# Optimization experiments

Hardware: AMD Instinct MI355X
Metric: run time of the kernel (lower is better)

## Reference

```python
import jax, jax.numpy as jnp
import numpy as np

B, N, F_IN, F_OUT = 8, 2048, 256, 256
H, D = 8, 32
LN_EPS = 1e-5


def setup_inputs() -> dict:
    key = jax.random.key(0)
    ks = jax.random.split(key, 8)
    s = 1.0 / np.sqrt(F_IN)
    so = 1.0 / np.sqrt(H * D)
    return {
        "x": jax.random.normal(ks[0], (B, N, F_IN), dtype=jnp.float32),
        "adj": jax.random.randint(ks[1], (B, N, N), 0, 2, dtype=jnp.int32),
        "Wq": jax.random.uniform(ks[2], (F_IN, H * D), jnp.float32, -s, s),
        "bq": jnp.zeros((H * D,), jnp.float32),
        "Wk": jax.random.uniform(ks[3], (F_IN, H * D), jnp.float32, -s, s),
        "bk": jnp.zeros((H * D,), jnp.float32),
        "Wv": jax.random.uniform(ks[4], (F_IN, H * D), jnp.float32, -s, s),
        "bv": jnp.zeros((H * D,), jnp.float32),
        "Wo": jax.random.uniform(ks[5], (H * D, F_OUT), jnp.float32, -so, so),
        "bo": jnp.zeros((F_OUT,), jnp.float32),
        "gamma": jnp.ones((F_OUT,), jnp.float32),
        "beta": jnp.zeros((F_OUT,), jnp.float32),
    }


def reference(x, adj, Wq, bq, Wk, bk, Wv, bv, Wo, bo, gamma, beta):
    b, n, _ = x.shape
    # QKV projections -> [B, H, N, D]
    q = (x @ Wq + bq).reshape(b, n, H, D).transpose(0, 2, 1, 3)
    k = (x @ Wk + bk).reshape(b, n, H, D).transpose(0, 2, 1, 3)
    v = (x @ Wv + bv).reshape(b, n, H, D).transpose(0, 2, 1, 3)
    # masked attention scores [B, H, N, N]
    scores = jnp.einsum('bhqd,bhkd->bhqk', q, k) / np.sqrt(D).astype(np.float32)
    scores = jnp.where(adj[:, None, :, :] == 0, -jnp.inf, scores)
    attn = jax.nn.softmax(scores, axis=-1)
    # dropout layers are identity in eval mode
    out = jnp.einsum('bhqk,bhkd->bhqd', attn, v)
    out = out.transpose(0, 2, 1, 3).reshape(b, n, H * D)
    out = out @ Wo + bo
    # LayerNorm
    mu = out.mean(-1, keepdims=True)
    var = out.var(-1, keepdims=True)
    out = (out - mu) * jax.lax.rsqrt(var + LN_EPS) * gamma + beta
    return out, attn.mean(axis=1)
```

## Files before the change

### kernel.cpp

```cpp
#include <hip/hip_runtime.h>


typedef __attribute__((ext_vector_type(8))) short short8;
typedef __attribute__((ext_vector_type(4))) float f32x4;
typedef __attribute__((ext_vector_type(4))) unsigned short us4;
typedef unsigned short u16;
typedef unsigned int u32;

#define SC2 0.25503486127240555f
#define MS2 28.853900817779268f

__device__ __forceinline__ float b2f(u16 u) {
  union { u32 i; float f; } v; v.i = ((u32)u) << 16; return v.f;
}
__device__ __forceinline__ u16 f2b(float f) {
  union { float f; u32 i; } v; v.f = f;
  u32 r = v.i + 0x7FFFu + ((v.i >> 16) & 1u);
  return (u16)(r >> 16);
}
__device__ __forceinline__ u16 f2br(float f) {
  union { float f; u32 i; } v; v.f = f;
  return (u16)((v.i + 0x8000u) >> 16);
}

__global__ __launch_bounds__(256) void k_pack(const int* __restrict__ adj,
                                              u32* __restrict__ packed) {
  unsigned int i = blockIdx.x * 256u + threadIdx.x;
  unsigned long long m = __ballot(adj[i] != 0);
  int lane = threadIdx.x & 63;
  if (lane == 0)       packed[i >> 5] = (u32)m;
  else if (lane == 32) packed[i >> 5] = (u32)(m >> 32);
}

__global__ __launch_bounds__(256) void k_transpose4(
    const float* __restrict__ w0, const float* __restrict__ w1,
    const float* __restrict__ w2, const float* __restrict__ w3,
    u16* __restrict__ o0, u16* __restrict__ o1,
    u16* __restrict__ o2, u16* __restrict__ o3) {
  const float* in; u16* out;
  int z = blockIdx.z;
  if (z == 0) { in = w0; out = o0; }
  else if (z == 1) { in = w1; out = o1; }
  else if (z == 2) { in = w2; out = o2; }
  else { in = w3; out = o3; }
  __shared__ u16 t[32][33];
  int tx = threadIdx.x & 31, ty = threadIdx.x >> 5;
  int x0 = blockIdx.x * 32, y0 = blockIdx.y * 32;
  for (int j = 0; j < 32; j += 8)
    t[ty + j][tx] = f2b(in[(y0 + ty + j) * 256 + x0 + tx]);
  __syncthreads();
  for (int j = 0; j < 32; j += 8) out[(x0 + ty + j) * 256 + y0 + tx] = t[tx][ty + j];
}

__global__ __launch_bounds__(256) void k_qkv(
    const float* __restrict__ x, const u16* __restrict__ wt,
    const float* __restrict__ bq, const float* __restrict__ bk,
    const float* __restrict__ bv,
    u16* __restrict__ qw, u16* __restrict__ kw, u16* __restrict__ vt) {
  int l = threadIdx.x & 63, w = threadIdx.x >> 6;
  int lr = l & 15, lg = l >> 4;
  int row0 = blockIdx.y * 64 + w * 16;
  int c0 = blockIdx.x * 64;
  f32x4 acc[4] = {};
  const float* xr = x + (size_t)(row0 + lr) * 256 + lg * 8;
  const u16* wr = wt + (c0 + lr) * 256 + lg * 8;
  for (int k0 = 0; k0 < 256; k0 += 32) {
    f32x4 f0 = *(const f32x4*)(xr + k0);
    f32x4 f1 = *(const f32x4*)(xr + k0 + 4);
    short8 a;
    a[0] = (short)f2b(f0[0]); a[1] = (short)f2b(f0[1]);
    a[2] = (short)f2b(f0[2]); a[3] = (short)f2b(f0[3]);
    a[4] = (short)f2b(f1[0]); a[5] = (short)f2b(f1[1]);
    a[6] = (short)f2b(f1[2]); a[7] = (short)f2b(f1[3]);
#pragma unroll
    for (int ct = 0; ct < 4; ct++) {
      short8 bb = *(const short8*)(wr + ct * 16 * 256 + k0);
      acc[ct] = __builtin_amdgcn_mfma_f32_16x16x32_bf16(a, bb, acc[ct], 0, 0, 0);
    }
  }
  int mtx = blockIdx.x >> 2;
  const float* bias = (mtx == 0) ? bq : ((mtx == 1) ? bk : bv);
  int b = row0 >> 11, nbase = row0 & 2047;
#pragma unroll
  for (int ct = 0; ct < 4; ct++) {
    int cc = (c0 + ct * 16 + lr) & 255;
    int h = cc >> 5, d = cc & 31;
    float bs = bias[cc];
    if (mtx < 2) {
      u16* dst = (mtx == 0) ? qw : kw;
#pragma unroll
      for (int rr = 0; rr < 4; rr++) {
        int n = nbase + lg * 4 + rr;
        dst[((b * 8 + h) * 2048 + n) * 32 + d] = f2b(acc[ct][rr] + bs);
      }
    } else {
      us4 pk;
#pragma unroll
      for (int rr = 0; rr < 4; rr++) pk[rr] = f2b(acc[ct][rr] + bs);
      *(us4*)(vt + (size_t)((b * 8 + h) * 32 + d) * 2048 + nbase + lg * 4) = pk;
    }
  }
}

__global__ __launch_bounds__(256) void k_pass1(
    const u16* __restrict__ qw, const u16* __restrict__ kw,
    const u32* __restrict__ packed, float* __restrict__ lsl2) {
  int l = threadIdx.x & 63, w = threadIdx.x >> 6;
  int lr = l & 15, lg = l >> 4;
  int wid = blockIdx.x * 4 + w;
  int b = wid >> 9, h = (wid >> 6) & 7, q0 = (wid & 63) * 32;
  const u16* qb = qw + (size_t)((b * 8 + h) * 2048) * 32;
  const u16* kb = kw + (size_t)((b * 8 + h) * 2048) * 32;
  short8 qf0 = *(const short8*)(qb + (q0 + lr) * 32 + lg * 8);
  short8 qf1 = *(const short8*)(qb + (q0 + 16 + lr) * 32 + lg * 8);
  const u32* pkb = packed + (size_t)(b * 2048 + q0) * 64;
  float ls0 = 0.f, ls1 = 0.f;
#pragma unroll 2
  for (int ch = 0; ch < 32; ch++) {
    uint2 m0 = *(const uint2*)(pkb + lr * 64 + ch * 2);
    uint2 m1 = *(const uint2*)(pkb + (16 + lr) * 64 + ch * 2);
#pragma unroll
    for (int j = 0; j < 4; j++) {
      short8 kf = *(const short8*)(kb + (size_t)(ch * 64 + j * 16 + lr) * 32 + lg * 8);
      f32x4 z = {};
      f32x4 s0 = __builtin_amdgcn_mfma_f32_16x16x32_bf16(kf, qf0, z, 0, 0, 0);
      f32x4 s1 = __builtin_amdgcn_mfma_f32_16x16x32_bf16(kf, qf1, z, 0, 0, 0);
      u32 w0 = ((j & 2) ? m0.y : m0.x) >> ((j & 1) * 16 + lg * 4);
      u32 w1 = ((j & 2) ? m1.y : m1.x) >> ((j & 1) * 16 + lg * 4);
#pragma unroll
      for (int rr = 0; rr < 4; rr++) {
        float e0 = __builtin_exp2f(fmaf(s0[rr], SC2, -MS2));
        float e1 = __builtin_exp2f(fmaf(s1[rr], SC2, -MS2));
        ls0 += ((w0 >> rr) & 1u) ? e0 : 0.0f;
        ls1 += ((w1 >> rr) & 1u) ? e1 : 0.0f;
      }
    }
  }
  ls0 += __shfl_xor(ls0, 16); ls0 += __shfl_xor(ls0, 32);
  ls1 += __shfl_xor(ls1, 16); ls1 += __shfl_xor(ls1, 32);
  if (l < 16) {
    float* lp = lsl2 + (size_t)(b * 8 + h) * 2048 + q0;
    lp[lr]      = -__log2f(fmaxf(ls0, 1e-30f));
    lp[16 + lr] = -__log2f(fmaxf(ls1, 1e-30f));
  }
}

__global__ __launch_bounds__(512) void k_pass2(
    const u16* __restrict__ qw, const u16* __restrict__ kw,
    const u16* __restrict__ vt, const u32* __restrict__ packed,
    const float* __restrict__ lsl2, u16* __restrict__ ao,
    float* __restrict__ out2) {
  __shared__ __align__(16) u16 P[2][8][2048];
  int l = threadIdx.x & 63, h = threadIdx.x >> 6;
  int lr = l & 15, lg = l >> 4;
  int b = blockIdx.y, q0 = blockIdx.x * 32;
  const u16* qb = qw + (size_t)((b * 8 + h) * 2048 + q0) * 32;
  const u16* kb = kw + (size_t)((b * 8 + h) * 2048) * 32;
  const u16* vb = vt + (size_t)((b * 8 + h) * 32) * 2048;
  short8 qf0 = *(const short8*)(qb + lr * 32 + lg * 8);
  short8 qf1 = *(const short8*)(qb + (16 + lr) * 32 + lg * 8);
  float lil0 = lsl2[(size_t)(b * 8 + h) * 2048 + q0 + lr] - MS2;
  float lil1 = lsl2[(size_t)(b * 8 + h) * 2048 + q0 + 16 + lr] - MS2;
  f32x4 acc[2][2] = {};
  const u32* pkb = packed + (size_t)(b * 2048 + q0) * 64;
  for (int ch = 0; ch < 32; ch++) {
    u16* Pt = &P[ch & 1][h][0];
    uint2 m0 = *(const uint2*)(pkb + lr * 64 + ch * 2);
    uint2 m1 = *(const uint2*)(pkb + (16 + lr) * 64 + ch * 2);
#pragma unroll
    for (int j = 0; j < 4; j++) {
      short8 kf = *(const short8*)(kb + (size_t)(ch * 64 + j * 16 + lr) * 32 + lg * 8);
      f32x4 z = {};
      f32x4 s0 = __builtin_amdgcn_mfma_f32_16x16x32_bf16(kf, qf0, z, 0, 0, 0);
      f32x4 s1 = __builtin_amdgcn_mfma_f32_16x16x32_bf16(kf, qf1, z, 0, 0, 0);
      u32 w0 = ((j & 2) ? m0.y : m0.x) >> ((j & 1) * 16 + lg * 4);
      u32 w1 = ((j & 2) ? m1.y : m1.x) >> ((j & 1) * 16 + lg * 4);
      us4 p0, p1;
#pragma unroll
      for (int rr = 0; rr < 4; rr++) {
        float e0 = __builtin_exp2f(fmaf(s0[rr], SC2, lil0));
        float e1 = __builtin_exp2f(fmaf(s1[rr], SC2, lil1));
        p0[rr] = f2br(((w0 >> rr) & 1u) ? e0 : 0.0f);
        p1[rr] = f2br(((w1 >> rr) & 1u) ? e1 : 0.0f);
      }
      int slot = 2 * j + (lg >> 1), offs = (lg & 1) * 4;
      *(us4*)(Pt + lr * 64 + ((slot ^ (lr & 7)) << 3) + offs) = p0;
      *(us4*)(Pt + (16 + lr) * 64 + ((slot ^ (lr & 7)) << 3) + offs) = p1;
    }
#pragma unroll
    for (int k2 = 0; k2 < 2; k2++) {
      short8 pa0 = *(const short8*)(Pt + lr * 64 +
                      (((k2 * 4 + lg) ^ (lr & 7)) << 3));
      short8 pa1 = *(const short8*)(Pt + (16 + lr) * 64 +
                      (((k2 * 4 + lg) ^ (lr & 7)) << 3));
#pragma unroll
      for (int dt = 0; dt < 2; dt++) {
        short8 vf = *(const short8*)(vb + (size_t)(dt * 16 + lr) * 2048 +
                                     ch * 64 + k2 * 32 + lg * 8);
        acc[0][dt] = __builtin_amdgcn_mfma_f32_16x16x32_bf16(pa0, vf, acc[0][dt], 0, 0, 0);
        acc[1][dt] = __builtin_amdgcn_mfma_f32_16x16x32_bf16(pa1, vf, acc[1][dt], 0, 0, 0);
      }
    }
    __syncthreads();
    {
      int t = threadIdx.x;
      int r = t >> 4, c4 = t & 15;
      int addr = r * 64 + (((c4 >> 1) ^ (r & 7)) << 3) + (c4 & 1) * 4;
      float s0 = 0.f, s1 = 0.f, s2 = 0.f, s3 = 0.f;
#pragma unroll
      for (int w8 = 0; w8 < 8; w8++) {
        us4 v = *(const us4*)&P[ch & 1][w8][addr];
        s0 += b2f(v[0]); s1 += b2f(v[1]); s2 += b2f(v[2]); s3 += b2f(v[3]);
      }
      f32x4 o;
      o[0] = s0 * 0.125f; o[1] = s1 * 0.125f;
      o[2] = s2 * 0.125f; o[3] = s3 * 0.125f;
      *(f32x4*)(out2 + (size_t)(b * 2048 + q0 + r) * 2048 + ch * 64 + c4 * 4) = o;
    }
  }
#pragma unroll
  for (int qs = 0; qs < 2; qs++)
#pragma unroll
    for (int dt = 0; dt < 2; dt++)
#pragma unroll
      for (int rr = 0; rr < 4; rr++) {
        int n = q0 + qs * 16 + lg * 4 + rr;
        ao[(size_t)(b * 2048 + n) * 256 + h * 32 + dt * 16 + lr] =
            f2b(acc[qs][dt][rr]);
      }
}

__global__ __launch_bounds__(256) void k_oproj(
    const u16* __restrict__ ao, const u16* __restrict__ wto,
    const float* __restrict__ bo, const float* __restrict__ gamma,
    const float* __restrict__ beta, float* __restrict__ out) {
  int l = threadIdx.x & 63, w = threadIdx.x >> 6;
  int lr = l & 15, lg = l >> 4;
  int row0 = blockIdx.x * 64 + w * 16;
  f32x4 acc[16] = {};
  const u16* ar = ao + (size_t)(row0 + lr) * 256 + lg * 8;
  const u16* wr = wto + lr * 256 + lg * 8;
  for (int k0 = 0; k0 < 256; k0 += 32) {
    short8 a = *(const short8*)(ar + k0);
#pragma unroll
    for (int ct = 0; ct < 16; ct++) {
      short8 bb = *(const short8*)(wr + ct * 16 * 256 + k0);
      acc[ct] = __builtin_amdgcn_mfma_f32_16x16x32_bf16(a, bb, acc[ct], 0, 0, 0);
    }
  }
  float sum[4] = {0, 0, 0, 0}, sq[4] = {0, 0, 0, 0};
#pragma unroll
  for (int ct = 0; ct < 16; ct++) {
    float bs = bo[ct * 16 + lr];
#pragma unroll
    for (int rr = 0; rr < 4; rr++) {
      float v = acc[ct][rr] + bs;
      acc[ct][rr] = v;
      sum[rr] += v; sq[rr] += v * v;
    }
  }
#pragma unroll
  for (int rr = 0; rr < 4; rr++) {
    float s = sum[rr], q = sq[rr];
    s += __shfl_xor(s, 1); s += __shfl_xor(s, 2);
    s += __shfl_xor(s, 4); s += __shfl_xor(s, 8);
    q += __shfl_xor(q, 1); q += __shfl_xor(q, 2);
    q += __shfl_xor(q, 4); q += __shfl_xor(q, 8);
    float mu = s * (1.0f / 256.0f);
    float var = fmaxf(q * (1.0f / 256.0f) - mu * mu, 0.0f);
    sum[rr] = mu;
    sq[rr] = rsqrtf(var + 1e-5f);
  }
#pragma unroll
  for (int ct = 0; ct < 16; ct++) {
    float g = gamma[ct * 16 + lr], be = beta[ct * 16 + lr];
#pragma unroll
    for (int rr = 0; rr < 4; rr++) {
      int n = row0 + lg * 4 + rr;
      out[(size_t)n * 256 + ct * 16 + lr] =
          ((acc[ct][rr] - sum[rr]) * sq[rr]) * g + be;
    }
  }
}

extern "C" void kernel_launch(void* const* d_in, const int* in_sizes, int n_in,
                              void* d_out, int out_size, void* d_ws, size_t ws_size,
                              hipStream_t stream) {
  const float* x    = (const float*)d_in[0];
  const int*   adj  = (const int*)d_in[1];
  const float* Wq   = (const float*)d_in[2];
  const float* bq   = (const float*)d_in[3];
  const float* Wk   = (const float*)d_in[4];
  const float* bk   = (const float*)d_in[5];
  const float* Wv   = (const float*)d_in[6];
  const float* bv   = (const float*)d_in[7];
  const float* Wo   = (const float*)d_in[8];
  const float* bo   = (const float*)d_in[9];
  const float* gamma= (const float*)d_in[10];
  const float* beta = (const float*)d_in[11];

  char* ws = (char*)d_ws;
  u16* wtq = (u16*)(ws + 0);
  u16* wtk = (u16*)(ws + 131072);
  u16* wtv = (u16*)(ws + 262144);
  u16* wto = (u16*)(ws + 393216);
  u16* qw  = (u16*)(ws + 524288);
  u16* kw  = (u16*)(ws + 8912896);
  u16* vt  = (u16*)(ws + 17301504);
  u16* ao  = (u16*)(ws + 25690112);
  u32* pk  = (u32*)(ws + 34078720);
  float* lsl2 = (float*)(ws + 38273024);

  float* out  = (float*)d_out;
  float* out2 = out + (size_t)8 * 2048 * 256;

  k_pack<<<dim3(131072), dim3(256), 0, stream>>>(adj, pk);
  k_transpose4<<<dim3(8, 8, 4), dim3(256), 0, stream>>>(Wq, Wk, Wv, Wo,
                                                        wtq, wtk, wtv, wto);
  k_qkv<<<dim3(12, 256), dim3(256), 0, stream>>>(x, wtq, bq, bk, bv, qw, kw, vt);
  k_pass1<<<dim3(1024), dim3(256), 0, stream>>>(qw, kw, pk, lsl2);
  k_pass2<<<dim3(64, 8), dim3(512), 0, stream>>>(qw, kw, vt, pk, lsl2, ao, out2);
  k_oproj<<<dim3(256), dim3(256), 0, stream>>>(ao, wto, bo, gamma, beta, out);
}
```

Before: 408.9 us.

## Fuse softmax row-sum pass into attention kernel and batch adjacency packing

The separate row-sum kernel is merged into the attention kernel, so each block computes its log-sum before producing probabilities. This removes a launch and the intermediate log-sum buffer. The adjacency pack kernel now processes 64 tiles per block, cutting block count, and the manual bf16 rounding helpers are replaced by the native bf16 cast. The fused kernel runs the first pass with fewer, larger blocks, which may reduce latency hiding.

```diff
diff --git a/kernel.cpp b/kernel.cpp
--- a/kernel.cpp
+++ b/kernel.cpp
@@ -13,23 +13,21 @@
 __device__ __forceinline__ float b2f(u16 u) {
   union { u32 i; float f; } v; v.i = ((u32)u) << 16; return v.f;
 }
-__device__ __forceinline__ u16 f2b(float f) {
-  union { float f; u32 i; } v; v.f = f;
-  u32 r = v.i + 0x7FFFu + ((v.i >> 16) & 1u);
-  return (u16)(r >> 16);
-}
-__device__ __forceinline__ u16 f2br(float f) {
-  union { float f; u32 i; } v; v.f = f;
-  return (u16)((v.i + 0x8000u) >> 16);
+__device__ __forceinline__ u16 cvt(float f) {
+  __bf16 h = (__bf16)f;
+  union { __bf16 h; u16 u; } v; v.h = h; return v.u;
 }
 
 __global__ __launch_bounds__(256) void k_pack(const int* __restrict__ adj,
                                               u32* __restrict__ packed) {
-  unsigned int i = blockIdx.x * 256u + threadIdx.x;
-  unsigned long long m = __ballot(adj[i] != 0);
   int lane = threadIdx.x & 63;
-  if (lane == 0)       packed[i >> 5] = (u32)m;
-  else if (lane == 32) packed[i >> 5] = (u32)(m >> 32);
+#pragma unroll 4
+  for (int it = 0; it < 64; it++) {
+    unsigned int i = (blockIdx.x * 64u + it) * 256u + threadIdx.x;
+    unsigned long long m = __ballot(adj[i] != 0);
+    if (lane == 0)       packed[i >> 5] = (u32)m;
+    else if (lane == 32) packed[i >> 5] = (u32)(m >> 32);
+  }
 }
 
 __global__ __launch_bounds__(256) void k_transpose4(
@@ -47,7 +45,7 @@
   int tx = threadIdx.x & 31, ty = threadIdx.x >> 5;
   int x0 = blockIdx.x * 32, y0 = blockIdx.y * 32;
   for (int j = 0; j < 32; j += 8)
-    t[ty + j][tx] = f2b(in[(y0 + ty + j) * 256 + x0 + tx]);
+    t[ty + j][tx] = cvt(in[(y0 + ty + j) * 256 + x0 + tx]);
   __syncthreads();
   for (int j = 0; j < 32; j += 8) out[(x0 + ty + j) * 256 + y0 + tx] = t[tx][ty + j];
 }
@@ -68,10 +66,10 @@
     f32x4 f0 = *(const f32x4*)(xr + k0);
     f32x4 f1 = *(const f32x4*)(xr + k0 + 4);
     short8 a;
-    a[0] = (short)f2b(f0[0]); a[1] = (short)f2b(f0[1]);
-    a[2] = (short)f2b(f0[2]); a[3] = (short)f2b(f0[3]);
-    a[4] = (short)f2b(f1[0]); a[5] = (short)f2b(f1[1]);
-    a[6] = (short)f2b(f1[2]); a[7] = (short)f2b(f1[3]);
+    a[0] = (short)cvt(f0[0]); a[1] = (short)cvt(f0[1]);
+    a[2] = (short)cvt(f0[2]); a[3] = (short)cvt(f0[3]);
+    a[4] = (short)cvt(f1[0]); a[5] = (short)cvt(f1[1]);
+    a[6] = (short)cvt(f1[2]); a[7] = (short)cvt(f1[3]);
 #pragma unroll
     for (int ct = 0; ct < 4; ct++) {
       short8 bb = *(const short8*)(wr + ct * 16 * 256 + k0);
@@ -91,65 +89,21 @@
 #pragma unroll
       for (int rr = 0; rr < 4; rr++) {
         int n = nbase + lg * 4 + rr;
-        dst[((b * 8 + h) * 2048 + n) * 32 + d] = f2b(acc[ct][rr] + bs);
+        dst[((b * 8 + h) * 2048 + n) * 32 + d] = cvt(acc[ct][rr] + bs);
       }
     } else {
       us4 pk;
 #pragma unroll
-      for (int rr = 0; rr < 4; rr++) pk[rr] = f2b(acc[ct][rr] + bs);
+      for (int rr = 0; rr < 4; rr++) pk[rr] = cvt(acc[ct][rr] + bs);
       *(us4*)(vt + (size_t)((b * 8 + h) * 32 + d) * 2048 + nbase + lg * 4) = pk;
     }
   }
 }
 
-__global__ __launch_bounds__(256) void k_pass1(
-    const u16* __restrict__ qw, const u16* __restrict__ kw,
-    const u32* __restrict__ packed, float* __restrict__ lsl2) {
-  int l = threadIdx.x & 63, w = threadIdx.x >> 6;
-  int lr = l & 15, lg = l >> 4;
-  int wid = blockIdx.x * 4 + w;
-  int b = wid >> 9, h = (wid >> 6) & 7, q0 = (wid & 63) * 32;
-  const u16* qb = qw + (size_t)((b * 8 + h) * 2048) * 32;
-  const u16* kb = kw + (size_t)((b * 8 + h) * 2048) * 32;
-  short8 qf0 = *(const short8*)(qb + (q0 + lr) * 32 + lg * 8);
-  short8 qf1 = *(const short8*)(qb + (q0 + 16 + lr) * 32 + lg * 8);
-  const u32* pkb = packed + (size_t)(b * 2048 + q0) * 64;
-  float ls0 = 0.f, ls1 = 0.f;
-#pragma unroll 2
-  for (int ch = 0; ch < 32; ch++) {
-    uint2 m0 = *(const uint2*)(pkb + lr * 64 + ch * 2);
-    uint2 m1 = *(const uint2*)(pkb + (16 + lr) * 64 + ch * 2);
-#pragma unroll
-    for (int j = 0; j < 4; j++) {
-      short8 kf = *(const short8*)(kb + (size_t)(ch * 64 + j * 16 + lr) * 32 + lg * 8);
-      f32x4 z = {};
-      f32x4 s0 = __builtin_amdgcn_mfma_f32_16x16x32_bf16(kf, qf0, z, 0, 0, 0);
-      f32x4 s1 = __builtin_amdgcn_mfma_f32_16x16x32_bf16(kf, qf1, z, 0, 0, 0);
-      u32 w0 = ((j & 2) ? m0.y : m0.x) >> ((j & 1) * 16 + lg * 4);
-      u32 w1 = ((j & 2) ? m1.y : m1.x) >> ((j & 1) * 16 + lg * 4);
-#pragma unroll
-      for (int rr = 0; rr < 4; rr++) {
-        float e0 = __builtin_exp2f(fmaf(s0[rr], SC2, -MS2));
-        float e1 = __builtin_exp2f(fmaf(s1[rr], SC2, -MS2));
-        ls0 += ((w0 >> rr) & 1u) ? e0 : 0.0f;
-        ls1 += ((w1 >> rr) & 1u) ? e1 : 0.0f;
-      }
-    }
-  }
-  ls0 += __shfl_xor(ls0, 16); ls0 += __shfl_xor(ls0, 32);
-  ls1 += __shfl_xor(ls1, 16); ls1 += __shfl_xor(ls1, 32);
-  if (l < 16) {
-    float* lp = lsl2 + (size_t)(b * 8 + h) * 2048 + q0;
-    lp[lr]      = -__log2f(fmaxf(ls0, 1e-30f));
-    lp[16 + lr] = -__log2f(fmaxf(ls1, 1e-30f));
-  }
-}
-
-__global__ __launch_bounds__(512) void k_pass2(
+__global__ __launch_bounds__(512) void k_attn(
     const u16* __restrict__ qw, const u16* __restrict__ kw,
     const u16* __restrict__ vt, const u32* __restrict__ packed,
-    const float* __restrict__ lsl2, u16* __restrict__ ao,
-    float* __restrict__ out2) {
+    u16* __restrict__ ao, float* __restrict__ out2) {
   __shared__ __align__(16) u16 P[2][8][2048];
   int l = threadIdx.x & 63, h = threadIdx.x >> 6;
   int lr = l & 15, lg = l >> 4;
@@ -159,10 +113,36 @@
   const u16* vb = vt + (size_t)((b * 8 + h) * 32) * 2048;
   short8 qf0 = *(const short8*)(qb + lr * 32 + lg * 8);
   short8 qf1 = *(const short8*)(qb + (16 + lr) * 32 + lg * 8);
-  float lil0 = lsl2[(size_t)(b * 8 + h) * 2048 + q0 + lr] - MS2;
-  float lil1 = lsl2[(size_t)(b * 8 + h) * 2048 + q0 + 16 + lr] - MS2;
+  const u32* pkb = packed + (size_t)(b * 2048 + q0) * 64;
+
+  float ls0 = 0.f, ls1 = 0.f;
+#pragma unroll 2
+  for (int ch = 0; ch < 32; ch++) {
+    uint2 m0 = *(const uint2*)(pkb + lr * 64 + ch * 2);
+    uint2 m1 = *(const uint2*)(pkb + (16 + lr) * 64 + ch * 2);
+#pragma unroll
+    for (int j = 0; j < 4; j++) {
+      short8 kf = *(const short8*)(kb + (size_t)(ch * 64 + j * 16 + lr) * 32 + lg * 8);
+      f32x4 z = {};
+      f32x4 s0 = __builtin_amdgcn_mfma_f32_16x16x32_bf16(kf, qf0, z, 0, 0, 0);
+      f32x4 s1 = __builtin_amdgcn_mfma_f32_16x16x32_bf16(kf, qf1, z, 0, 0, 0);
+      u32 w0 = ((j & 2) ? m0.y : m0.x) >> ((j & 1) * 16 + lg * 4);
+      u32 w1 = ((j & 2) ? m1.y : m1.x) >> ((j & 1) * 16 + lg * 4);
+#pragma unroll
+      for (int rr = 0; rr < 4; rr++) {
+        float e0 = __builtin_exp2f(fmaf(s0[rr], SC2, -MS2));
+        float e1 = __builtin_exp2f(fmaf(s1[rr], SC2, -MS2));
+        ls0 += ((w0 >> rr) & 1u) ? e0 : 0.0f;
+        ls1 += ((w1 >> rr) & 1u) ? e1 : 0.0f;
+      }
+    }
+  }
+  ls0 += __shfl_xor(ls0, 16); ls0 += __shfl_xor(ls0, 32);
+  ls1 += __shfl_xor(ls1, 16); ls1 += __shfl_xor(ls1, 32);
+  float lil0 = -__log2f(fmaxf(ls0, 1e-30f)) - MS2;
+  float lil1 = -__log2f(fmaxf(ls1, 1e-30f)) - MS2;
+
   f32x4 acc[2][2] = {};
-  const u32* pkb = packed + (size_t)(b * 2048 + q0) * 64;
   for (int ch = 0; ch < 32; ch++) {
     u16* Pt = &P[ch & 1][h][0];
     uint2 m0 = *(const uint2*)(pkb + lr * 64 + ch * 2);
@@ -180,8 +160,8 @@
       for (int rr = 0; rr < 4; rr++) {
         float e0 = __builtin_exp2f(fmaf(s0[rr], SC2, lil0));
         float e1 = __builtin_exp2f(fmaf(s1[rr], SC2, lil1));
-        p0[rr] = f2br(((w0 >> rr) & 1u) ? e0 : 0.0f);
-        p1[rr] = f2br(((w1 >> rr) & 1u) ? e1 : 0.0f);
+        p0[rr] = cvt(((w0 >> rr) & 1u) ? e0 : 0.0f);
+        p1[rr] = cvt(((w1 >> rr) & 1u) ? e1 : 0.0f);
       }
       int slot = 2 * j + (lg >> 1), offs = (lg & 1) * 4;
       *(us4*)(Pt + lr * 64 + ((slot ^ (lr & 7)) << 3) + offs) = p0;
@@ -226,7 +206,7 @@
       for (int rr = 0; rr < 4; rr++) {
         int n = q0 + qs * 16 + lg * 4 + rr;
         ao[(size_t)(b * 2048 + n) * 256 + h * 32 + dt * 16 + lr] =
-            f2b(acc[qs][dt][rr]);
+            cvt(acc[qs][dt][rr]);
       }
 }
 
@@ -309,16 +289,14 @@
   u16* vt  = (u16*)(ws + 17301504);
   u16* ao  = (u16*)(ws + 25690112);
   u32* pk  = (u32*)(ws + 34078720);
-  float* lsl2 = (float*)(ws + 38273024);
 
   float* out  = (float*)d_out;
   float* out2 = out + (size_t)8 * 2048 * 256;
 
-  k_pack<<<dim3(131072), dim3(256), 0, stream>>>(adj, pk);
+  k_pack<<<dim3(2048), dim3(256), 0, stream>>>(adj, pk);
   k_transpose4<<<dim3(8, 8, 4), dim3(256), 0, stream>>>(Wq, Wk, Wv, Wo,
                                                         wtq, wtk, wtv, wto);
   k_qkv<<<dim3(12, 256), dim3(256), 0, stream>>>(x, wtq, bq, bk, bv, qw, kw, vt);
-  k_pass1<<<dim3(1024), dim3(256), 0, stream>>>(qw, kw, pk, lsl2);
-  k_pass2<<<dim3(64, 8), dim3(512), 0, stream>>>(qw, kw, vt, pk, lsl2, ao, out2);
+  k_attn<<<dim3(64, 8), dim3(512), 0, stream>>>(qw, kw, vt, pk, ao, out2);
   k_oproj<<<dim3(256), dim3(256), 0, stream>>>(ao, wto, bo, gamma, beta, out);
 }
```

Result: no change. 405.0 us (-1.0%).
